# Kernel tuning notes

Hardware: AMD Instinct MI355X
Metric: run time of the kernel (lower is better)

## Reference

```python
import jax, jax.numpy as jnp
import numpy as np

B, L, D = 8, 4096, 768
NC = L          # compact slots == max_len (compact_tensors_batch = zeros_like(tensors_batch))
N_CH = L // 2   # actual chunk-id range


def setup_inputs() -> dict:
    key = jax.random.key(0)
    k1, k2, k3, k4, k5 = jax.random.split(key, 5)
    tensors_batch = jax.random.normal(k1, (B, L, D), jnp.float32)
    # sorted segment ids -> contiguous ragged chunks per row; skipped ids are empty slots
    seg_ids = jnp.sort(jax.random.randint(k2, (B, L), 0, N_CH), axis=-1).astype(jnp.int32)
    # chunk-constant masks (the module asserts any()==all() within a chunk)
    pad_len = jax.random.randint(k3, (B, 1), N_CH // 2, N_CH)
    chunk_pad = (jnp.arange(N_CH)[None, :] < pad_len).astype(jnp.int32)          # 1 = real token
    chunk_reg = jax.random.randint(k4, (B, N_CH), 0, 2).astype(jnp.int32)
    chunk_sp = jnp.broadcast_to((jnp.arange(N_CH)[None, :] >= N_CH // 2).astype(jnp.int32), (B, N_CH))
    padding_mask = jnp.take_along_axis(chunk_pad, seg_ids, axis=1)
    regular_tokens_mask = jnp.take_along_axis(chunk_reg, seg_ids, axis=1)
    seq_pair_mask = jnp.take_along_axis(chunk_sp, seg_ids, axis=1)
    # gen_net params: mean-pool over chunk -> Linear(D,D) -> tanh
    W = jax.random.normal(k5, (D, D), jnp.float32) / np.float32(np.sqrt(D))
    b = jnp.zeros((D,), jnp.float32)
    return {"tensors_batch": tensors_batch, "seg_ids": seg_ids,
            "padding_mask": padding_mask, "regular_tokens_mask": regular_tokens_mask,
            "seq_pair_mask": seq_pair_mask, "W": W, "b": b}


def _seg_sum(x, sid):
    return jax.ops.segment_sum(x, sid, num_segments=NC)


def reference(tensors_batch, seg_ids, padding_mask, regular_tokens_mask, seq_pair_mask, W, b):
    f32 = jnp.float32
    counts = jax.vmap(_seg_sum)(jnp.ones((B, L), f32), seg_ids)                  # [B,NC]
    sums = jax.vmap(_seg_sum)(tensors_batch, seg_ids)                            # [B,NC,D]
    mean = sums / jnp.maximum(counts, 1.0)[..., None]
    joint = jnp.tanh(jnp.einsum('bnd,de->bne', mean, W) + b)                     # gen_net
    compact = jnp.where(counts[..., None] > 0, joint, 0.0)                       # scatter into zeros
    pad_any = jax.vmap(_seg_sum)(padding_mask.astype(f32), seg_ids) > 0
    reg_any = jax.vmap(_seg_sum)(regular_tokens_mask.astype(f32), seg_ids) > 0
    sp_sum = jax.vmap(_seg_sum)(seq_pair_mask.astype(f32), seg_ids)
    sp_all = (sp_sum == counts) & (counts > 0)                                   # prod != 0 over chunk
    mask_padding = pad_any.astype(jnp.int32)
    mask_regular = reg_any.astype(jnp.int32)
    mask_seq_pair = jnp.where(mask_padding == 0, -1, sp_all.astype(jnp.int32))
    # column trimming (mask_padding.sum(0)==0) is data-dependent-shape; zero instead of slice
    keep = (mask_padding.sum(axis=0) > 0)                                        # [NC]
    compact_out = compact * keep[None, :, None]
    mask_padding_o = mask_padding * keep[None, :]
    mask_regular_o = mask_regular * keep[None, :]
    mask_seq_pair_o = mask_seq_pair * keep[None, :]
    compression_rate = jnp.sum(mask_regular_o).astype(f32) / jnp.sum(regular_tokens_mask).astype(f32)
    return compact_out, mask_padding_o, mask_regular_o, mask_seq_pair_o, compression_rate
```

## Files before the change

kernel.cpp:

```cpp
#include <hip/hip_runtime.h>
#include <math.h>

#define B_   8
#define L_   4096
#define D_   768
#define NC_  4096
#define NCH_ 2048
#define M_   (B_*NC_)
#define MC_  (B_*NCH_)
#define NKT_ 24
#define META_BLOCKS 128
#define WPREP_BLOCKS 144
#define GEMM_BLOCKS 256

typedef __attribute__((ext_vector_type(8))) short short8;
typedef __attribute__((ext_vector_type(4))) float f32x4;
typedef unsigned int u32;
typedef unsigned short u16;

__device__ __forceinline__ void gload16(const void* g, void* l) {
    __builtin_amdgcn_global_load_lds((const __attribute__((address_space(1))) u32*)g,
                                     (__attribute__((address_space(3))) u32*)l, 16, 0, 0);
}

__device__ __forceinline__ u16 f2bf(float f) {
    union { float f; u32 u; } v; v.f = f;
    u32 r = v.u + 0x7fffu + ((v.u >> 16) & 1u);
    return (u16)(r >> 16);
}

__device__ __forceinline__ float tanh_fast(float x) {
    float e = __builtin_amdgcn_exp2f(x * 2.885390081777927f);
    return 1.f - 2.f * __builtin_amdgcn_rcpf(e + 1.f);
}

__device__ __forceinline__ int lower_bound(const int* __restrict__ a, int lo, int hi, int v) {
    while (lo < hi) {
        int mid = (lo + hi) >> 1;
        if (a[mid] < v) lo = mid + 1; else hi = mid;
    }
    return lo;
}

__global__ void prep_kernel(const int* __restrict__ seg,
                            const int* __restrict__ padm,
                            const int* __restrict__ regm,
                            const int* __restrict__ spm,
                            const float* __restrict__ Wm,
                            u16* __restrict__ wt,
                            int* __restrict__ stA, int* __restrict__ cntA,
                            int* __restrict__ act,
                            float* __restrict__ out_mp, float* __restrict__ out_mr,
                            float* __restrict__ out_sp,
                            float2* __restrict__ partials) {
    __shared__ float shm[64 * 65 + 8];
    int blk = blockIdx.x;
    int t = threadIdx.x;
    if (blk >= META_BLOCKS) {
        int wb = blk - META_BLOCKS;
        int bk = wb % 12, bn = wb / 12;
        int k0 = bk * 64, n0 = bn * 64;
        int ln = t & 63, lw = t >> 6;
        #pragma unroll
        for (int p = 0; p < 16; ++p) {
            int kl = lw + p * 4;
            shm[kl * 65 + ln] = Wm[(size_t)(k0 + kl) * D_ + n0 + ln];
        }
        __syncthreads();
        #pragma unroll
        for (int p = 0; p < 16; ++p) {
            int nl = lw + p * 4;
            wt[(size_t)(n0 + nl) * D_ + k0 + ln] = f2bf(shm[ln * 65 + nl]);
        }
        return;
    }
    int idx = blk * 256 + t;
    int c = idx >> 3, b = idx & 7;
    const int* row = seg + b * L_;
    int s = lower_bound(row, 0, L_, c);
    int e = __shfl_down(s, 8);
    if ((t & 63) >= 56) e = lower_bound(row, s, L_, c + 1);
    int cnt = e - s;
    int mp = 0, mr = 0;
    if (cnt > 0) { mp = padm[b * L_ + s]; mr = regm[b * L_ + s]; }
    int sp = (mp == 0) ? -1 : spm[b * L_ + s];
    int k = mp;
    k |= __shfl_xor(k, 1);
    k |= __shfl_xor(k, 2);
    k |= __shfl_xor(k, 4);
    k = k ? 1 : 0;
    out_mp[b * NC_ + c] = (float)mp;
    out_mr[b * NC_ + c] = (float)(k ? mr : 0);
    out_sp[b * NC_ + c] = (float)(k ? sp : 0);
    if (c < NCH_) {
        int mc = b * NCH_ + c;
        stA[mc] = s;
        cntA[mc] = cnt;
        act[mc] = (k && cnt > 0) ? 1 : 0;
    }
    float numP = (float)(k * mr);
    float denP = (float)(cnt * mr);
    #pragma unroll
    for (int off = 32; off; off >>= 1) {
        numP += __shfl_down(numP, off);
        denP += __shfl_down(denP, off);
    }
    __syncthreads();
    if ((t & 63) == 0) { shm[(t >> 6) * 2] = numP; shm[(t >> 6) * 2 + 1] = denP; }
    __syncthreads();
    if (t == 0)
        partials[blk] = make_float2(shm[0] + shm[2] + shm[4] + shm[6],
                                    shm[1] + shm[3] + shm[5] + shm[7]);
}

__global__ __launch_bounds__(512, 1) void fused_kernel(
        const float* __restrict__ x,
        const int* __restrict__ stA, const int* __restrict__ cntA,
        const u16* __restrict__ wt,
        const float* __restrict__ bias,
        const int* __restrict__ act,
        const float2* __restrict__ partials,
        float* __restrict__ out, float* __restrict__ rateOut) {
    __shared__ char sB[3 * 49152];
    __shared__ char sA[2 * 4096];
    __shared__ int sMeta[128];
    __shared__ float rb[4];
    int bid = blockIdx.x;
    int t = threadIdx.x;
    if (bid >= GEMM_BLOCKS) {
        float n = 0.f, d = 0.f;
        if (t < META_BLOCKS) { float2 p = partials[t]; n = p.x; d = p.y; }
        #pragma unroll
        for (int off = 32; off; off >>= 1) { n += __shfl_down(n, off); d += __shfl_down(d, off); }
        if (t < META_BLOCKS && (t & 63) == 0) { rb[(t >> 6) * 2] = n; rb[(t >> 6) * 2 + 1] = d; }
        __syncthreads();
        if (t == 0) rateOut[0] = (rb[0] + rb[2]) / (rb[1] + rb[3]);
        return;
    }
    int wg = (bid & 7) * 32 + (bid >> 3);
    int m0 = wg << 6;
    int b = m0 >> 11;
    int lane = t & 63, w = t >> 6;

    if (t < 64) { sMeta[t] = stA[m0 + t]; sMeta[64 + t] = cntA[m0 + t]; }

    const char* bT = (const char*)wt;
    const float* xb = x + (size_t)b * L_ * D_;

    int srcB[8];
    #pragma unroll
    for (int j = 0; j < 8; ++j) {
        int i = t + j * 384;
        int r = i >> 2, s = i & 3;
        srcB[j] = r * 1536 + ((s ^ ((r ^ (r >> 2)) & 3)) << 4);
    }
    int dbB = w * 1024;

    int aoff[4], boff[8];
    #pragma unroll
    for (int f = 0; f < 4; ++f) {
        int r = f * 16 + (lane & 15);
        aoff[f] = r * 64 + ((((lane >> 4)) ^ ((r ^ (r >> 2)) & 3)) << 4);
    }
    #pragma unroll
    for (int g = 0; g < 8; ++g) {
        int r = w * 128 + g * 16 + (lane & 15);
        boff[g] = r * 64 + ((((lane >> 4)) ^ ((r ^ (r >> 2)) & 3)) << 4);
    }

    if (w < 6) {
        #pragma unroll
        for (int p = 0; p < 2; ++p)
            #pragma unroll
            for (int j = 0; j < 8; ++j)
                gload16(bT + srcB[j] + (p << 6), sB + p * 49152 + j * 6144 + dbB);
    }
    __syncthreads();

    auto produceA = [&](int kt) {
        int pt = t - 384;
        int r = pt >> 1, h = pt & 1;
        int st = sMeta[r], cnt = sMeta[64 + r];
        const float* base = xb + (size_t)st * D_ + (kt << 5) + h * 16;
        float a16[16];
        #pragma unroll
        for (int i = 0; i < 16; ++i) a16[i] = 0.f;
        int tk = 0;
        for (; tk + 2 <= cnt; tk += 2) {
            const float* p0 = base + (size_t)tk * D_;
            const float* p1 = p0 + D_;
            #pragma unroll
            for (int i = 0; i < 16; ++i) a16[i] += p0[i] + p1[i];
        }
        if (tk < cnt) {
            const float* p0 = base + (size_t)tk * D_;
            #pragma unroll
            for (int i = 0; i < 16; ++i) a16[i] += p0[i];
        }
        float inv = (cnt > 0) ? 1.f / (float)cnt : 0.f;
        short8 v1, v2;
        #pragma unroll
        for (int i = 0; i < 8; ++i) v1[i] = (short)f2bf(a16[i] * inv);
        #pragma unroll
        for (int i = 0; i < 8; ++i) v2[i] = (short)f2bf(a16[8 + i] * inv);
        char* slice = sA + ((kt & 1) << 12);
        int sw = (r ^ (r >> 2)) & 3;
        *(short8*)(slice + r * 64 + (((2 * h) ^ sw) << 4)) = v1;
        *(short8*)(slice + r * 64 + (((2 * h + 1) ^ sw) << 4)) = v2;
    };

    f32x4 acc[4][8] = {};

    if (w >= 6) produceA(0);

    #pragma unroll 1
    for (int kt = 0; kt < NKT_; ++kt) {
        if (w < 6) {
            if (kt < NKT_ - 1) asm volatile("s_waitcnt vmcnt(8)" ::: "memory");
            else               asm volatile("s_waitcnt vmcnt(0)" ::: "memory");
        } else {
            asm volatile("s_waitcnt lgkmcnt(0)" ::: "memory");
        }
        __builtin_amdgcn_s_barrier();
        __builtin_amdgcn_sched_barrier(0);
        if (w < 6) {
            const char* curA = sA + ((kt & 1) << 12);
            const char* curB = sB + (kt % 3) * 49152;
            short8 afr[4], bfr[8];
            #pragma unroll
            for (int f = 0; f < 4; ++f) afr[f] = *(const short8*)(curA + aoff[f]);
            #pragma unroll
            for (int g = 0; g < 8; ++g) bfr[g] = *(const short8*)(curB + boff[g]);
            if (kt + 2 < NKT_) {
                int kof = (kt + 2) << 6;
                char* d = sB + ((kt + 2) % 3) * 49152;
                #pragma unroll
                for (int j = 0; j < 8; ++j)
                    gload16(bT + srcB[j] + kof, d + j * 6144 + dbB);
            }
            __builtin_amdgcn_s_setprio(1);
            #pragma unroll
            for (int f = 0; f < 4; ++f)
                #pragma unroll
                for (int g = 0; g < 8; ++g)
                    acc[f][g] = __builtin_amdgcn_mfma_f32_16x16x32_bf16(
                        afr[f], bfr[g], acc[f][g], 0, 0, 0);
            __builtin_amdgcn_s_setprio(0);
        } else {
            if (kt + 1 < NKT_) produceA(kt + 1);
        }
        __builtin_amdgcn_sched_barrier(0);
    }

    if (w < 6) {
        int ncol[8]; float bs[8];
        #pragma unroll
        for (int g = 0; g < 8; ++g) {
            ncol[g] = w * 128 + g * 16 + (lane & 15);
            bs[g] = bias[ncol[g]];
        }
        #pragma unroll
        for (int f = 0; f < 4; ++f) {
            int rbase = m0 + f * 16 + ((lane >> 4) << 2);
            #pragma unroll
            for (int q = 0; q < 4; ++q) {
                int mc = rbase + q;
                int av = act[mc];
                int gr = mc + ((mc >> 11) << 11);
                size_t orow = (size_t)gr * D_;
                #pragma unroll
                for (int g = 0; g < 8; ++g) {
                    float v = av ? tanh_fast(acc[f][g][q] + bs[g]) : 0.f;
                    out[orow + ncol[g]] = v;
                }
            }
        }
    }

    {
        int sp = wg >> 5;
        size_t zb = (size_t)(sp * 4096 + 2048) * 3072 + (size_t)(wg & 31) * 196608;
        float4* pz = (float4*)((char*)out + zb);
        float4 zz = make_float4(0.f, 0.f, 0.f, 0.f);
        #pragma unroll
        for (int i = 0; i < 24; ++i) pz[t + i * 512] = zz;
    }
}

extern "C" void kernel_launch(void* const* d_in, const int* in_sizes, int n_in,
                              void* d_out, int out_size, void* d_ws, size_t ws_size,
                              hipStream_t stream) {
    const float* x    = (const float*)d_in[0];
    const int*   seg  = (const int*)d_in[1];
    const int*   padm = (const int*)d_in[2];
    const int*   regm = (const int*)d_in[3];
    const int*   spm  = (const int*)d_in[4];
    const float* Wm   = (const float*)d_in[5];
    const float* bias = (const float*)d_in[6];
    float* out = (float*)d_out;

    char* ws = (char*)d_ws;
    float2* partials = (float2*)ws;
    int* stA  = (int*)(ws + 1024);
    int* cntA = stA + MC_;
    int* act  = cntA + MC_;
    u16* wt   = (u16*)(act + MC_);

    float* out_mp = out + (size_t)M_ * D_;
    float* out_mr = out_mp + M_;
    float* out_sp = out_mr + M_;
    float* out_rate = out_sp + M_;

    prep_kernel<<<META_BLOCKS + WPREP_BLOCKS, 256, 0, stream>>>(
        seg, padm, regm, spm, Wm, wt, stA, cntA, act,
        out_mp, out_mr, out_sp, partials);
    fused_kernel<<<GEMM_BLOCKS + 1, 512, 0, stream>>>(
        x, stA, cntA, wt, bias, act, partials, out, out_rate);
}
```

Baseline: 89.37 us.

## Shrink row tile to 32 and pool all A rows up front with every wave

The fused pool+GEMM kernel now uses 32-row tiles, which doubles the block count to 512. All 8 waves first mean-pool the whole 32x768 A tile into LDS with coalesced float4 loads, and only then run the GEMM. This replaces the warp-specialized producer/consumer pipeline, and W is double-buffered instead of triple-buffered. The aim is better CU coverage on a 256-CU part and higher bandwidth for the gather. The cost is that each block reloads all of W twice as often, and the GEMM loop waits on vmcnt(0) every step with less prefetch depth.

```diff
diff --git a/kernel.cpp b/kernel.cpp
--- a/kernel.cpp
+++ b/kernel.cpp
@@ -11,7 +11,7 @@
 #define NKT_ 24
 #define META_BLOCKS 128
 #define WPREP_BLOCKS 144
-#define GEMM_BLOCKS 256
+#define FUSED_BLOCKS 512
 
 typedef __attribute__((ext_vector_type(8))) short short8;
 typedef __attribute__((ext_vector_type(4))) float f32x4;
@@ -98,7 +98,7 @@
         cntA[mc] = cnt;
         act[mc] = (k && cnt > 0) ? 1 : 0;
     }
-    float numP = (float)(k * mr);
+    float numP = (float)(k ? mr : 0);
     float denP = (float)(cnt * mr);
     #pragma unroll
     for (int off = 32; off; off >>= 1) {
@@ -113,7 +113,7 @@
                                     shm[1] + shm[3] + shm[5] + shm[7]);
 }
 
-__global__ __launch_bounds__(512, 1) void fused_kernel(
+__global__ __launch_bounds__(512, 1) void fused32_kernel(
         const float* __restrict__ x,
         const int* __restrict__ stA, const int* __restrict__ cntA,
         const u16* __restrict__ wt,
@@ -121,13 +121,13 @@
         const int* __restrict__ act,
         const float2* __restrict__ partials,
         float* __restrict__ out, float* __restrict__ rateOut) {
-    __shared__ char sB[3 * 49152];
-    __shared__ char sA[2 * 4096];
-    __shared__ int sMeta[128];
+    __shared__ char sAlds[49152];
+    __shared__ char sB[2 * 49152];
+    __shared__ int sMeta[64];
     __shared__ float rb[4];
     int bid = blockIdx.x;
     int t = threadIdx.x;
-    if (bid >= GEMM_BLOCKS) {
+    if (bid >= FUSED_BLOCKS) {
         float n = 0.f, d = 0.f;
         if (t < META_BLOCKS) { float2 p = partials[t]; n = p.x; d = p.y; }
         #pragma unroll
@@ -137,153 +137,135 @@
         if (t == 0) rateOut[0] = (rb[0] + rb[2]) / (rb[1] + rb[3]);
         return;
     }
-    int wg = (bid & 7) * 32 + (bid >> 3);
-    int m0 = wg << 6;
+    int wg = bid;
+    int m0 = wg << 5;
     int b = m0 >> 11;
     int lane = t & 63, w = t >> 6;
 
-    if (t < 64) { sMeta[t] = stA[m0 + t]; sMeta[64 + t] = cntA[m0 + t]; }
+    if (t < 32) { sMeta[t] = stA[m0 + t]; sMeta[32 + t] = cntA[m0 + t]; }
 
     const char* bT = (const char*)wt;
-    const float* xb = x + (size_t)b * L_ * D_;
-
-    int srcB[8];
-    #pragma unroll
-    for (int j = 0; j < 8; ++j) {
-        int i = t + j * 384;
+    int srcB[6];
+    #pragma unroll
+    for (int j = 0; j < 6; ++j) {
+        int i = t + j * 512;
         int r = i >> 2, s = i & 3;
         srcB[j] = r * 1536 + ((s ^ ((r ^ (r >> 2)) & 3)) << 4);
     }
     int dbB = w * 1024;
 
-    int aoff[4], boff[8];
-    #pragma unroll
-    for (int f = 0; f < 4; ++f) {
+    __syncthreads();
+
+    #pragma unroll
+    for (int j = 0; j < 6; ++j)
+        gload16(bT + srcB[j], sB + j * 8192 + dbB);
+
+    const float* xb = x + (size_t)b * L_ * D_;
+    #pragma unroll 1
+    for (int i = 0; i < 4; ++i) {
+        int rr = (w << 2) + i;
+        int st = sMeta[rr], cnt = sMeta[32 + rr];
+        float a0=0.f,a1=0.f,a2=0.f,a3=0.f,a4=0.f,a5=0.f,
+              a6=0.f,a7=0.f,a8=0.f,a9=0.f,a10=0.f,a11=0.f;
+        const float4* base = (const float4*)(xb + (size_t)st * D_) + lane;
+        for (int tk = 0; tk < cnt; ++tk) {
+            const float4* p = base + (size_t)tk * 192;
+            float4 v0 = p[0], v1 = p[64], v2 = p[128];
+            a0 += v0.x; a1 += v0.y; a2  += v0.z; a3  += v0.w;
+            a4 += v1.x; a5 += v1.y; a6  += v1.z; a7  += v1.w;
+            a8 += v2.x; a9 += v2.y; a10 += v2.z; a11 += v2.w;
+        }
+        float inv = (cnt > 0) ? 1.f / (float)cnt : 0.f;
+        int sw = (rr ^ (rr >> 2)) & 3;
+        int kt0 = lane >> 3;
+        int bofs = rr * 64 + ((((lane & 7) >> 1) ^ sw) << 4) + (lane & 1) * 8;
+        u32 lo, hi;
+        lo = (u32)f2bf(a0*inv) | ((u32)f2bf(a1*inv) << 16);
+        hi = (u32)f2bf(a2*inv) | ((u32)f2bf(a3*inv) << 16);
+        *(uint2*)(sAlds + kt0 * 2048 + bofs) = make_uint2(lo, hi);
+        lo = (u32)f2bf(a4*inv) | ((u32)f2bf(a5*inv) << 16);
+        hi = (u32)f2bf(a6*inv) | ((u32)f2bf(a7*inv) << 16);
+        *(uint2*)(sAlds + (8 + kt0) * 2048 + bofs) = make_uint2(lo, hi);
+        lo = (u32)f2bf(a8*inv) | ((u32)f2bf(a9*inv) << 16);
+        hi = (u32)f2bf(a10*inv) | ((u32)f2bf(a11*inv) << 16);
+        *(uint2*)(sAlds + (16 + kt0) * 2048 + bofs) = make_uint2(lo, hi);
+    }
+    __syncthreads();
+
+    int aoff[2], boff[6];
+    #pragma unroll
+    for (int f = 0; f < 2; ++f) {
         int r = f * 16 + (lane & 15);
         aoff[f] = r * 64 + ((((lane >> 4)) ^ ((r ^ (r >> 2)) & 3)) << 4);
     }
     #pragma unroll
-    for (int g = 0; g < 8; ++g) {
-        int r = w * 128 + g * 16 + (lane & 15);
+    for (int g = 0; g < 6; ++g) {
+        int r = w * 96 + g * 16 + (lane & 15);
         boff[g] = r * 64 + ((((lane >> 4)) ^ ((r ^ (r >> 2)) & 3)) << 4);
     }
 
-    if (w < 6) {
-        #pragma unroll
-        for (int p = 0; p < 2; ++p)
-            #pragma unroll
-            for (int j = 0; j < 8; ++j)
-                gload16(bT + srcB[j] + (p << 6), sB + p * 49152 + j * 6144 + dbB);
-    }
-    __syncthreads();
-
-    auto produceA = [&](int kt) {
-        int pt = t - 384;
-        int r = pt >> 1, h = pt & 1;
-        int st = sMeta[r], cnt = sMeta[64 + r];
-        const float* base = xb + (size_t)st * D_ + (kt << 5) + h * 16;
-        float a16[16];
-        #pragma unroll
-        for (int i = 0; i < 16; ++i) a16[i] = 0.f;
-        int tk = 0;
-        for (; tk + 2 <= cnt; tk += 2) {
-            const float* p0 = base + (size_t)tk * D_;
-            const float* p1 = p0 + D_;
-            #pragma unroll
-            for (int i = 0; i < 16; ++i) a16[i] += p0[i] + p1[i];
-        }
-        if (tk < cnt) {
-            const float* p0 = base + (size_t)tk * D_;
-            #pragma unroll
-            for (int i = 0; i < 16; ++i) a16[i] += p0[i];
-        }
-        float inv = (cnt > 0) ? 1.f / (float)cnt : 0.f;
-        short8 v1, v2;
-        #pragma unroll
-        for (int i = 0; i < 8; ++i) v1[i] = (short)f2bf(a16[i] * inv);
-        #pragma unroll
-        for (int i = 0; i < 8; ++i) v2[i] = (short)f2bf(a16[8 + i] * inv);
-        char* slice = sA + ((kt & 1) << 12);
-        int sw = (r ^ (r >> 2)) & 3;
-        *(short8*)(slice + r * 64 + (((2 * h) ^ sw) << 4)) = v1;
-        *(short8*)(slice + r * 64 + (((2 * h + 1) ^ sw) << 4)) = v2;
-    };
-
-    f32x4 acc[4][8] = {};
-
-    if (w >= 6) produceA(0);
+    f32x4 acc[2][6] = {};
 
     #pragma unroll 1
     for (int kt = 0; kt < NKT_; ++kt) {
-        if (w < 6) {
-            if (kt < NKT_ - 1) asm volatile("s_waitcnt vmcnt(8)" ::: "memory");
-            else               asm volatile("s_waitcnt vmcnt(0)" ::: "memory");
-        } else {
-            asm volatile("s_waitcnt lgkmcnt(0)" ::: "memory");
-        }
+        asm volatile("s_waitcnt vmcnt(0)" ::: "memory");
         __builtin_amdgcn_s_barrier();
         __builtin_amdgcn_sched_barrier(0);
-        if (w < 6) {
-            const char* curA = sA + ((kt & 1) << 12);
-            const char* curB = sB + (kt % 3) * 49152;
-            short8 afr[4], bfr[8];
+        const char* curA = sAlds + kt * 2048;
+        const char* curB = sB + (kt & 1) * 49152;
+        if (kt + 1 < NKT_) {
+            int kof = (kt + 1) << 6;
+            char* d = sB + ((kt + 1) & 1) * 49152;
             #pragma unroll
-            for (int f = 0; f < 4; ++f) afr[f] = *(const short8*)(curA + aoff[f]);
+            for (int j = 0; j < 6; ++j)
+                gload16(bT + srcB[j] + kof, d + j * 8192 + dbB);
+        }
+        short8 afr[2], bfr[6];
+        #pragma unroll
+        for (int f = 0; f < 2; ++f) afr[f] = *(const short8*)(curA + aoff[f]);
+        #pragma unroll
+        for (int g = 0; g < 6; ++g) bfr[g] = *(const short8*)(curB + boff[g]);
+        __builtin_amdgcn_s_setprio(1);
+        #pragma unroll
+        for (int f = 0; f < 2; ++f)
             #pragma unroll
-            for (int g = 0; g < 8; ++g) bfr[g] = *(const short8*)(curB + boff[g]);
-            if (kt + 2 < NKT_) {
-                int kof = (kt + 2) << 6;
-                char* d = sB + ((kt + 2) % 3) * 49152;
-                #pragma unroll
-                for (int j = 0; j < 8; ++j)
-                    gload16(bT + srcB[j] + kof, d + j * 6144 + dbB);
+            for (int g = 0; g < 6; ++g)
+                acc[f][g] = __builtin_amdgcn_mfma_f32_16x16x32_bf16(
+                    afr[f], bfr[g], acc[f][g], 0, 0, 0);
+        __builtin_amdgcn_s_setprio(0);
+        __builtin_amdgcn_sched_barrier(0);
+    }
+
+    int ncol[6]; float bs[6];
+    #pragma unroll
+    for (int g = 0; g < 6; ++g) {
+        ncol[g] = w * 96 + g * 16 + (lane & 15);
+        bs[g] = bias[ncol[g]];
+    }
+    #pragma unroll
+    for (int f = 0; f < 2; ++f) {
+        int rbase = m0 + f * 16 + ((lane >> 4) << 2);
+        #pragma unroll
+        for (int q = 0; q < 4; ++q) {
+            int mc = rbase + q;
+            int av = act[mc];
+            int gr = mc + ((mc >> 11) << 11);
+            size_t orow = (size_t)gr * D_;
+            #pragma unroll
+            for (int g = 0; g < 6; ++g) {
+                float v = av ? tanh_fast(acc[f][g][q] + bs[g]) : 0.f;
+                out[orow + ncol[g]] = v;
             }
-            __builtin_amdgcn_s_setprio(1);
-            #pragma unroll
-            for (int f = 0; f < 4; ++f)
-                #pragma unroll
-                for (int g = 0; g < 8; ++g)
-                    acc[f][g] = __builtin_amdgcn_mfma_f32_16x16x32_bf16(
-                        afr[f], bfr[g], acc[f][g], 0, 0, 0);
-            __builtin_amdgcn_s_setprio(0);
-        } else {
-            if (kt + 1 < NKT_) produceA(kt + 1);
-        }
-        __builtin_amdgcn_sched_barrier(0);
-    }
-
-    if (w < 6) {
-        int ncol[8]; float bs[8];
-        #pragma unroll
-        for (int g = 0; g < 8; ++g) {
-            ncol[g] = w * 128 + g * 16 + (lane & 15);
-            bs[g] = bias[ncol[g]];
-        }
-        #pragma unroll
-        for (int f = 0; f < 4; ++f) {
-            int rbase = m0 + f * 16 + ((lane >> 4) << 2);
-            #pragma unroll
-            for (int q = 0; q < 4; ++q) {
-                int mc = rbase + q;
-                int av = act[mc];
-                int gr = mc + ((mc >> 11) << 11);
-                size_t orow = (size_t)gr * D_;
-                #pragma unroll
-                for (int g = 0; g < 8; ++g) {
-                    float v = av ? tanh_fast(acc[f][g][q] + bs[g]) : 0.f;
-                    out[orow + ncol[g]] = v;
-                }
-            }
         }
     }
 
     {
-        int sp = wg >> 5;
-        size_t zb = (size_t)(sp * 4096 + 2048) * 3072 + (size_t)(wg & 31) * 196608;
+        int sp = wg >> 6;
+        size_t zb = (size_t)(sp * 4096 + 2048) * 3072 + (size_t)(wg & 63) * 98304;
         float4* pz = (float4*)((char*)out + zb);
         float4 zz = make_float4(0.f, 0.f, 0.f, 0.f);
         #pragma unroll
-        for (int i = 0; i < 24; ++i) pz[t + i * 512] = zz;
+        for (int i = 0; i < 12; ++i) pz[t + i * 512] = zz;
     }
 }
 
@@ -314,6 +296,6 @@
     prep_kernel<<<META_BLOCKS + WPREP_BLOCKS, 256, 0, stream>>>(
         seg, padm, regm, spm, Wm, wt, stA, cntA, act,
         out_mp, out_mr, out_sp, partials);
-    fused_kernel<<<GEMM_BLOCKS + 1, 512, 0, stream>>>(
+    fused32_kernel<<<FUSED_BLOCKS + 1, 512, 0, stream>>>(
         x, stA, cntA, wt, bias, act, partials, out, out_rate);
 }
```

New measurement: 101.3 us. 1.13x slower.
